# Performance work log

Hardware: AMD Instinct MI355X
Metric: run time of the kernel (lower is better)

Reference implementation:

```python
import jax, jax.numpy as jnp
import numpy as np

N, E, G = 20000, 480000, 200
HID = 32  # hidden_channels


def setup_inputs() -> dict:
    key = jax.random.key(0)
    ks = jax.random.split(key, 40)
    rn = lambda k, shape, s=0.1: jax.random.normal(k, shape, jnp.float32) * s
    inp = {
        "x": jax.random.normal(ks[0], (N, 8), jnp.float32),
        "edge_index": jax.random.randint(ks[1], (2, E), 0, N),
        "edge_attr": jax.random.normal(ks[2], (E, 4), jnp.float32),
        "batch": jnp.sort(jax.random.randint(ks[3], (N,), 0, G)),
        "descriptors": jax.random.normal(ks[4], (G, 48), jnp.float32),
        # edge encoder Linear(4 -> 32)
        "We_enc": rn(ks[5], (4, HID)), "be_enc": rn(ks[6], (HID,)),
        # gat1: GATConv(8 -> 32, heads=4, concat)
        "W1": rn(ks[7], (8, 4 * HID)), "as1": rn(ks[8], (4, HID)), "ad1": rn(ks[9], (4, HID)), "b1": rn(ks[10], (4 * HID,)),
        # gat2: GATConv(128 -> 32, heads=4, concat, edge_dim=32)
        "W2": rn(ks[11], (4 * HID, 4 * HID)), "We2": rn(ks[12], (HID, 4 * HID)),
        "as2": rn(ks[13], (4, HID)), "ad2": rn(ks[14], (4, HID)), "ae2": rn(ks[15], (4, HID)), "b2": rn(ks[16], (4 * HID,)),
        # gat3
        "W3": rn(ks[17], (4 * HID, 4 * HID)), "We3": rn(ks[18], (HID, 4 * HID)),
        "as3": rn(ks[19], (4, HID)), "ad3": rn(ks[20], (4, HID)), "ae3": rn(ks[21], (4, HID)), "b3": rn(ks[22], (4 * HID,)),
        # gat4: heads=1, concat=False
        "W4": rn(ks[23], (4 * HID, HID)), "We4": rn(ks[24], (HID, HID)),
        "as4": rn(ks[25], (1, HID)), "ad4": rn(ks[26], (1, HID)), "ae4": rn(ks[27], (1, HID)), "b4": rn(ks[28], (HID,)),
        # descriptor net Linear(48 -> 32)
        "Wd": rn(ks[29], (48, HID)), "bd": rn(ks[30], (HID,)),
        # final Linear(64 -> 1)
        "Wl": rn(ks[31], (2 * HID, 1)), "bl": rn(ks[32], (1,)),
    }
    return inp


def _gat(x, src, dst, n, W, att_s, att_d, bias, heads, ch, concat, e=None, We=None, att_e=None):
    """PyG GATConv: add self-loops (edge fill='mean'), edge softmax over incoming edges."""
    loops = jnp.arange(n)
    if e is not None:
        cnt = jnp.zeros((n,), x.dtype).at[dst].add(1.0)
        loop_e = jnp.zeros((n, e.shape[1]), x.dtype).at[dst].add(e) / jnp.maximum(cnt, 1.0)[:, None]
        e = jnp.concatenate([e, loop_e], axis=0)  # [E+N, edge_dim]
    s = jnp.concatenate([src, loops])
    d = jnp.concatenate([dst, loops])
    h = (x @ W).reshape(n, heads, ch)                      # [N,H,C]
    a_s = (h * att_s).sum(-1)                              # [N,H]
    a_d = (h * att_d).sum(-1)
    alpha = a_s[s] + a_d[d]                                # [E+N,H]
    if e is not None:
        eh = (e @ We).reshape(-1, heads, ch)
        alpha = alpha + (eh * att_e).sum(-1)
    alpha = jax.nn.leaky_relu(alpha, 0.2)
    amax = jax.ops.segment_max(alpha, d, num_segments=n)
    ex = jnp.exp(alpha - amax[d])
    den = jax.ops.segment_sum(ex, d, num_segments=n)
    alpha = ex / (den[d] + 1e-16)
    out = jax.ops.segment_sum(alpha[:, :, None] * h[s], d, num_segments=n)  # [N,H,C]
    out = out.reshape(n, heads * ch) if concat else out.mean(axis=1)
    return out + bias


def reference(x, edge_index, edge_attr, batch, descriptors,
              We_enc, be_enc,
              W1, as1, ad1, b1,
              W2, We2, as2, ad2, ae2, b2,
              W3, We3, as3, ad3, ae3, b3,
              W4, We4, as4, ad4, ae4, b4,
              Wd, bd, Wl, bl):
    src, dst = edge_index[0], edge_index[1]
    n = x.shape[0]
    edge_emb = edge_attr @ We_enc + be_enc                # [E,32]
    h = jax.nn.relu(_gat(x, src, dst, n, W1, as1, ad1, b1, 4, HID, True))
    h = jax.nn.relu(_gat(h, src, dst, n, W2, as2, ad2, b2, 4, HID, True, edge_emb, We2, ae2))
    h = jax.nn.relu(_gat(h, src, dst, n, W3, as3, ad3, b3, 4, HID, True, edge_emb, We3, ae3))
    h = _gat(h, src, dst, n, W4, as4, ad4, b4, 1, HID, False, edge_emb, We4, ae4)  # [N,32]
    # global mean pool per graph
    g_sum = jax.ops.segment_sum(h, batch, num_segments=G)
    g_cnt = jax.ops.segment_sum(jnp.ones((n,), h.dtype), batch, num_segments=G)
    graph_emb = g_sum / jnp.maximum(g_cnt, 1.0)[:, None]  # [G,32]
    desc_emb = jax.nn.relu(descriptors @ Wd + bd)          # [G,32]
    combined = jnp.concatenate([graph_emb, desc_emb], axis=1)
    return jax.nn.sigmoid(combined @ Wl + bl).reshape(-1)  # [G]
```

## Files before the change

kernel.cpp:

```cpp
#include <hip/hip_runtime.h>
#include <hip/hip_bf16.h>
#include <math.h>

#define NN 20000
#define EE 480000
#define GG 200
#define CAP 96

typedef unsigned int uint32;

static __device__ inline unsigned short f2bf(float f) {
  __hip_bfloat16 h = __float2bfloat16(f);
  return *reinterpret_cast<const unsigned short*>(&h);
}
static __device__ inline float bf2f(unsigned short u) {
  return __uint_as_float(((uint32)u) << 16);
}
static __device__ inline float bf_lo(uint32 u) { return __uint_as_float(u << 16); }
static __device__ inline float bf_hi(uint32 u) { return __uint_as_float(u & 0xffff0000u); }
static __device__ inline uint32 pack2(float lo, float hi) {
  return ((uint32)f2bf(lo)) | (((uint32)f2bf(hi)) << 16);
}

#define HB ((EE + 255) / 256)
#define GB (NN / 16)

__global__ void histgemm1_kernel(const int* __restrict__ dst, int* __restrict__ cnt,
                                 const float* __restrict__ X, const float* __restrict__ W,
                                 const float* __restrict__ att_s, const float* __restrict__ att_d,
                                 __hip_bfloat16* __restrict__ H, float* __restrict__ a_s,
                                 float* __restrict__ a_d) {
  int tid = threadIdx.x;
  if (blockIdx.x < HB) {
    int i = blockIdx.x * 256 + tid;
    if (i < EE) atomicAdd(&cnt[dst[i]], 1);
    return;
  }
  __shared__ float xs[16][8];
  int row0 = (blockIdx.x - HB) * 16;
  if (tid < 128) xs[tid >> 3][tid & 7] = X[row0 * 8 + tid];
  __syncthreads();
  int c = tid & 127;
  int half = tid >> 7;
  float acc[8];
#pragma unroll
  for (int j = 0; j < 8; ++j) acc[j] = 0.f;
  for (int k = 0; k < 8; ++k) {
    float wv = W[k * 128 + c];
#pragma unroll
    for (int j = 0; j < 8; ++j) acc[j] = fmaf(xs[half * 8 + j][k], wv, acc[j]);
  }
  float asv = att_s[c], adv = att_d[c];
#pragma unroll
  for (int j = 0; j < 8; ++j) {
    int row = row0 + half * 8 + j;
    float vs = acc[j] * asv, vd = acc[j] * adv;
#pragma unroll
    for (int m = 16; m >= 1; m >>= 1) {
      vs += __shfl_xor(vs, m);
      vd += __shfl_xor(vd, m);
    }
    H[row * 128 + c] = __float2bfloat16(acc[j]);
    if ((tid & 31) == 0) {
      a_s[row * 4 + (c >> 5)] = vs;
      a_d[row * 4 + (c >> 5)] = vd;
    }
  }
}

#define NSCAN ((NN + 1023) / 1024)

__global__ void scan1_kernel(const int* __restrict__ cnt, int* __restrict__ row_ptr,
                             int* __restrict__ partial) {
  __shared__ int buf[1024];
  int t = threadIdx.x;
  int i = blockIdx.x * 1024 + t;
  int v = (i < NN) ? cnt[i] : 0;
  buf[t] = v;
  __syncthreads();
  for (int offd = 1; offd < 1024; offd <<= 1) {
    int tmp = (t >= offd) ? buf[t - offd] : 0;
    __syncthreads();
    buf[t] += tmp;
    __syncthreads();
  }
  if (i < NN) row_ptr[i + 1] = buf[t];
  if (t == 1023) partial[blockIdx.x] = buf[1023];
}

__global__ void scan23_kernel(int* __restrict__ row_ptr, const int* __restrict__ partial) {
  __shared__ int sc[NSCAN];
  int t = threadIdx.x;
  if (t < 64) {
    int v = (t < NSCAN) ? partial[t] : 0;
    for (int o = 1; o < 32; o <<= 1) {
      int u = __shfl_up(v, o);
      if (t >= o) v += u;
    }
    if (t < NSCAN) sc[t] = v;
  }
  __syncthreads();
  int i = blockIdx.x * 256 + t;
  if (i == 0) row_ptr[0] = 0;
  if (i >= 1 && i <= NN) {
    int b = (i - 1) >> 10;
    if (b > 0) row_ptr[i] += sc[b - 1];
  }
}

__global__ void scatter_kernel(const int* __restrict__ src, const int* __restrict__ dst,
                               const float* __restrict__ attr, const int* __restrict__ row_ptr,
                               int* __restrict__ pos, int* __restrict__ csr_src,
                               uint2* __restrict__ attr_pk) {
  int e = blockIdx.x * 256 + threadIdx.x;
  if (e >= EE) return;
  int d = dst[e];
  int p = row_ptr[d] + atomicAdd(&pos[d], 1);
  csr_src[p] = src[e];
  float4 a = ((const float4*)attr)[e];
  uint2 q;
  q.x = pack2(a.x, a.y);
  q.y = pack2(a.z, a.w);
  attr_pk[p] = q;
}

#define AMB ((NN + 255) / 256)

__global__ void aux_kernel(const int* __restrict__ row_ptr, const uint2* __restrict__ attr_pk,
                           float* __restrict__ mean_attr, const int* __restrict__ batch,
                           int* __restrict__ bound, const float* __restrict__ We_enc,
                           const float* __restrict__ be_enc, const float* __restrict__ We2,
                           const float* __restrict__ ae2, const float* __restrict__ We3,
                           const float* __restrict__ ae3, const float* __restrict__ We4,
                           const float* __restrict__ ae4, float* __restrict__ fold) {
  int b = blockIdx.x;
  int t = threadIdx.x;
  if (b < AMB) {
    int node = b * 256 + t;
    if (node < NN) {
      int p0 = row_ptr[node], p1 = row_ptr[node + 1];
      float s0 = 0.f, s1 = 0.f, s2 = 0.f, s3 = 0.f;
      for (int p = p0; p < p1; ++p) {
        uint2 q = attr_pk[p];
        s0 += bf_lo(q.x); s1 += bf_hi(q.x);
        s2 += bf_lo(q.y); s3 += bf_hi(q.y);
      }
      int deg = p1 - p0;
      float inv = 1.f / (float)(deg > 1 ? deg : 1);
      ((float4*)mean_attr)[node] = make_float4(s0 * inv, s1 * inv, s2 * inv, s3 * inv);
    }
    return;
  }
  if (b < 2 * AMB) {
    int i = (b - AMB) * 256 + t;
    if (i >= NN) return;
    int bc = batch[i];
    int bp = (i == 0) ? -1 : batch[i - 1];
    for (int g = bp + 1; g <= bc; ++g) bound[g] = i;
    if (i == NN - 1)
      for (int g = bc + 1; g <= GG; ++g) bound[g] = NN;
    return;
  }
  __shared__ float V[32 * 4];
  if (t < 128) {
    int k = t >> 2, h = t & 3;
    float s = 0.f;
    for (int c = 0; c < 32; ++c) s = fmaf(We2[k * 128 + h * 32 + c], ae2[h * 32 + c], s);
    V[k * 4 + h] = s;
  }
  __syncthreads();
  if (t < 16) {
    int i = t >> 2, h = t & 3;
    float s = 0.f;
    for (int k = 0; k < 32; ++k) s = fmaf(We_enc[i * 32 + k], V[k * 4 + h], s);
    fold[i * 4 + h] = s;
  } else if (t < 20) {
    int h = t - 16;
    float s = 0.f;
    for (int k = 0; k < 32; ++k) s = fmaf(be_enc[k], V[k * 4 + h], s);
    fold[16 + h] = s;
  }
  __syncthreads();
  if (t < 128) {
    int k = t >> 2, h = t & 3;
    float s = 0.f;
    for (int c = 0; c < 32; ++c) s = fmaf(We3[k * 128 + h * 32 + c], ae3[h * 32 + c], s);
    V[k * 4 + h] = s;
  }
  __syncthreads();
  if (t < 16) {
    int i = t >> 2, h = t & 3;
    float s = 0.f;
    for (int k = 0; k < 32; ++k) s = fmaf(We_enc[i * 32 + k], V[k * 4 + h], s);
    fold[20 + i * 4 + h] = s;
  } else if (t < 20) {
    int h = t - 16;
    float s = 0.f;
    for (int k = 0; k < 32; ++k) s = fmaf(be_enc[k], V[k * 4 + h], s);
    fold[36 + h] = s;
  }
  __syncthreads();
  if (t < 32) {
    float s = 0.f;
    for (int c = 0; c < 32; ++c) s = fmaf(We4[t * 32 + c], ae4[c], s);
    V[t] = s;
  }
  __syncthreads();
  if (t < 4) {
    float s = 0.f;
    for (int k = 0; k < 32; ++k) s = fmaf(We_enc[t * 32 + k], V[k], s);
    fold[40 + t] = s;
  } else if (t == 4) {
    float s = 0.f;
    for (int k = 0; k < 32; ++k) s = fmaf(be_enc[k], V[k], s);
    fold[44] = s;
  }
}

template <int COLS, int TR>
__global__ __launch_bounds__(256) void gemm2_kernel(const float* __restrict__ X,
                                                    const float* __restrict__ W,
                                                    const float* __restrict__ att_s,
                                                    const float* __restrict__ att_d,
                                                    __hip_bfloat16* __restrict__ H,
                                                    float* __restrict__ a_s,
                                                    float* __restrict__ a_d) {
  constexpr int K = 128;
  constexpr int HEADS = COLS / 32;
  constexpr int CG = COLS / 4;
  constexpr int RG = 256 / CG;
  constexpr int ROWS = RG * TR;
  __shared__ unsigned short ws[K * COLS];
  __shared__ float xs[ROWS * K];
  int tid = threadIdx.x;
  int row0 = blockIdx.x * ROWS;
  for (int i = tid * 4; i < K * COLS; i += 1024) {
    float4 wv = *(const float4*)&W[i];
    ushort4 u;
    u.x = f2bf(wv.x); u.y = f2bf(wv.y); u.z = f2bf(wv.z); u.w = f2bf(wv.w);
    *(ushort4*)&ws[i] = u;
  }
  for (int i = tid * 4; i < ROWS * K; i += 1024) {
    int grow = row0 + i / K;
    float4 v = make_float4(0.f, 0.f, 0.f, 0.f);
    if (grow < NN) v = *(const float4*)&X[(size_t)grow * K + (i & (K - 1))];
    *(float4*)&xs[i] = v;
  }
  __syncthreads();
  int cg = tid % CG, rg = tid / CG;
  int c0 = cg * 4, r0 = rg * TR;
  float acc[TR][4];
#pragma unroll
  for (int i = 0; i < TR; ++i)
#pragma unroll
    for (int j = 0; j < 4; ++j) acc[i][j] = 0.f;
  for (int k0 = 0; k0 < K; k0 += 4) {
    float w4[4][4];
#pragma unroll
    for (int j = 0; j < 4; ++j) {
      ushort4 u = *(ushort4*)&ws[(k0 + j) * COLS + c0];
      w4[j][0] = bf2f(u.x); w4[j][1] = bf2f(u.y); w4[j][2] = bf2f(u.z); w4[j][3] = bf2f(u.w);
    }
#pragma unroll
    for (int i = 0; i < TR; ++i) {
      float4 xv = *(float4*)&xs[(r0 + i) * K + k0];
#pragma unroll
      for (int j = 0; j < 4; ++j) {
        acc[i][j] = fmaf(xv.x, w4[0][j], acc[i][j]);
        acc[i][j] = fmaf(xv.y, w4[1][j], acc[i][j]);
        acc[i][j] = fmaf(xv.z, w4[2][j], acc[i][j]);
        acc[i][j] = fmaf(xv.w, w4[3][j], acc[i][j]);
      }
    }
  }
  float as4[4], ad4[4];
#pragma unroll
  for (int j = 0; j < 4; ++j) { as4[j] = att_s[c0 + j]; ad4[j] = att_d[c0 + j]; }
  int h = c0 >> 5;
#pragma unroll
  for (int i = 0; i < TR; ++i) {
    int row = row0 + r0 + i;
    ushort4 hv;
    hv.x = f2bf(acc[i][0]); hv.y = f2bf(acc[i][1]); hv.z = f2bf(acc[i][2]); hv.w = f2bf(acc[i][3]);
    if (row < NN) *(ushort4*)&H[(size_t)row * COLS + c0] = hv;
    float vs = 0.f, vd = 0.f;
#pragma unroll
    for (int j = 0; j < 4; ++j) {
      vs = fmaf(acc[i][j], as4[j], vs);
      vd = fmaf(acc[i][j], ad4[j], vd);
    }
#pragma unroll
    for (int m = 1; m <= 4; m <<= 1) {
      vs += __shfl_xor(vs, m);
      vd += __shfl_xor(vd, m);
    }
    if ((tid & 7) == 0 && row < NN) {
      a_s[row * HEADS + h] = vs;
      a_d[row * HEADS + h] = vd;
    }
  }
}

template <int HEADS, bool RELU, bool HAS_EDGE>
__global__ __launch_bounds__(256) void gat_agg5_kernel(
    const __hip_bfloat16* __restrict__ Hh, const float* __restrict__ a_s,
    const float* __restrict__ a_d, const uint2* __restrict__ attr_pk,
    const float* __restrict__ mean_attr, const float* __restrict__ foldM,
    const float* __restrict__ foldC, const int* __restrict__ row_ptr,
    const int* __restrict__ csr_src, const float* __restrict__ bias,
    float* __restrict__ out) {
  constexpr int COLS = HEADS * 32;
  constexpr int NL = COLS / 2;
  constexpr int NPB = 256 / NL;
  constexpr int EPP = 16;
  constexpr int JMAX = CAP / EPP;
  constexpr int EXS = CAP * HEADS + (HEADS == 1 ? 1 : 0);
  constexpr int SRS = CAP + (HEADS == 1 ? 1 : 0);

  __shared__ float ex_lds[NPB][EXS];
  __shared__ int src_lds[NPB][SRS];

  int tid = threadIdx.x;
  int ln = tid % NL;
  int nl = tid / NL;
  int node = blockIdx.x * NPB + nl;
  int p0 = row_ptr[node], p1 = row_ptr[node + 1];
  int deg = p1 - p0;
  int base = (tid & 63) & ~(NL - 1);
  const uint32* H32 = (const uint32*)Hh;
  int c = 2 * ln;
  int hc = (HEADS == 4) ? (c >> 5) : 0;

  if (deg > CAP) {
    float gm0 = 0.f, gm1 = 0.f, gm2 = 0.f, gm3 = 0.f, gc = 0.f;
    if (HAS_EDGE) {
      if (HEADS == 4) {
        gm0 = foldM[hc]; gm1 = foldM[4 + hc]; gm2 = foldM[8 + hc]; gm3 = foldM[12 + hc];
        gc = foldC[hc];
      } else {
        gm0 = foldM[0]; gm1 = foldM[1]; gm2 = foldM[2]; gm3 = foldM[3];
        gc = foldC[0];
      }
    }
    float adv = a_d[node * HEADS + hc];
    float al = a_s[node * HEADS + hc] + adv;
    if (HAS_EDGE) {
      float4 m4 = ((const float4*)mean_attr)[node];
      al += fmaf(m4.x, gm0, fmaf(m4.y, gm1, fmaf(m4.z, gm2, fmaf(m4.w, gm3, gc))));
    }
    al = al >= 0.f ? al : 0.2f * al;
    float m = al;
    for (int p = p0; p < p1; ++p) {
      int s = csr_src[p];
      float a = a_s[s * HEADS + hc] + adv;
      if (HAS_EDGE) {
        uint2 q = attr_pk[p];
        a += fmaf(bf_lo(q.x), gm0,
                  fmaf(bf_hi(q.x), gm1, fmaf(bf_lo(q.y), gm2, fmaf(bf_hi(q.y), gm3, gc))));
      }
      a = a >= 0.f ? a : 0.2f * a;
      m = fmaxf(m, a);
    }
    float e0 = __expf(al - m);
    float den = e0;
    uint32 u0 = H32[(size_t)node * NL + ln];
    float acc0 = e0 * bf_lo(u0), acc1 = e0 * bf_hi(u0);
    for (int p = p0; p < p1; ++p) {
      int s = csr_src[p];
      float a = a_s[s * HEADS + hc] + adv;
      if (HAS_EDGE) {
        uint2 q = attr_pk[p];
        a += fmaf(bf_lo(q.x), gm0,
                  fmaf(bf_hi(q.x), gm1, fmaf(bf_lo(q.y), gm2, fmaf(bf_hi(q.y), gm3, gc))));
      }
      a = a >= 0.f ? a : 0.2f * a;
      float ex = __expf(a - m);
      den += ex;
      uint32 u = H32[(size_t)s * NL + ln];
      acc0 = fmaf(ex, bf_lo(u), acc0);
      acc1 = fmaf(ex, bf_hi(u), acc1);
    }
    float inv = 1.f / (den + 1e-16f);
    float o0 = acc0 * inv + bias[c];
    float o1 = acc1 * inv + bias[c + 1];
    if (RELU) { o0 = fmaxf(o0, 0.f); o1 = fmaxf(o1, 0.f); }
    *(float2*)&out[(size_t)node * COLS + c] = make_float2(o0, o1);
    return;
  }

  int p_rel = ln / HEADS;
  int h = ln % HEADS;
  float adv = a_d[node * HEADS + h];
  float fm0 = 0.f, fm1 = 0.f, fm2 = 0.f, fm3 = 0.f, fc = 0.f;
  if (HAS_EDGE) {
    if (HEADS == 4) {
      fm0 = foldM[h]; fm1 = foldM[4 + h]; fm2 = foldM[8 + h]; fm3 = foldM[12 + h];
      fc = foldC[h];
    } else {
      fm0 = foldM[0]; fm1 = foldM[1]; fm2 = foldM[2]; fm3 = foldM[3];
      fc = foldC[0];
    }
  }

  float av[JMAX];
  float mpart = -1e30f;
#pragma unroll
  for (int j = 0; j < JMAX; ++j) {
    int pr = p_rel + j * EPP;
    av[j] = -1e30f;
    int s = 0;
    if (pr < deg) {
      int p = p0 + pr;
      s = csr_src[p];
      float a = a_s[s * HEADS + h] + adv;
      if (HAS_EDGE) {
        uint2 q = attr_pk[p];
        a += fmaf(bf_lo(q.x), fm0,
                  fmaf(bf_hi(q.x), fm1, fmaf(bf_lo(q.y), fm2, fmaf(bf_hi(q.y), fm3, fc))));
      }
      a = a >= 0.f ? a : 0.2f * a;
      av[j] = a;
      mpart = fmaxf(mpart, a);
    }
    if (HEADS == 1 || h == 0) src_lds[nl][pr] = s;
  }
  float al = -1e30f;
  if (p_rel == 0) {
    al = a_s[node * HEADS + h] + adv;
    if (HAS_EDGE && deg > 0) {
      float4 m4 = ((const float4*)mean_attr)[node];
      al += fmaf(m4.x, fm0, fmaf(m4.y, fm1, fmaf(m4.z, fm2, fmaf(m4.w, fm3, fc))));
    }
    al = al >= 0.f ? al : 0.2f * al;
    mpart = fmaxf(mpart, al);
  }
  float mfull = mpart;
#pragma unroll
  for (int m = HEADS; m < NL; m <<= 1) mfull = fmaxf(mfull, __shfl_xor(mfull, m));

  float dpart = 0.f;
#pragma unroll
  for (int j = 0; j < JMAX; ++j) {
    int pr = p_rel + j * EPP;
    float ex = __expf(av[j] - mfull);
    ex_lds[nl][pr * HEADS + h] = ex;
    dpart += ex;
  }
  float exl = 0.f;
  if (p_rel == 0) {
    exl = __expf(al - mfull);
    dpart += exl;
  }
  float den = dpart;
#pragma unroll
  for (int m = HEADS; m < NL; m <<= 1) den += __shfl_xor(den, m);

  float exl_c = __shfl(exl, base + hc);
  float den_c = __shfl(den, base + hc);
  uint32 u0 = H32[(size_t)node * NL + ln];
  float acc0 = exl_c * bf_lo(u0);
  float acc1 = exl_c * bf_hi(u0);
#pragma unroll
  for (int j = 0; j < JMAX; ++j) {
    if (j * EPP < deg) {
      float exv[EPP];
      int sval[EPP];
#pragma unroll
      for (int pp = 0; pp < EPP; ++pp) {
        int p = j * EPP + pp;
        sval[pp] = src_lds[nl][p];
        exv[pp] = ex_lds[nl][p * HEADS + hc];
      }
      uint32 uv[EPP];
#pragma unroll
      for (int pp = 0; pp < EPP; ++pp) uv[pp] = H32[(size_t)sval[pp] * NL + ln];
#pragma unroll
      for (int pp = 0; pp < EPP; ++pp) {
        acc0 = fmaf(exv[pp], bf_lo(uv[pp]), acc0);
        acc1 = fmaf(exv[pp], bf_hi(uv[pp]), acc1);
      }
    }
  }
  float inv = 1.f / (den_c + 1e-16f);
  float o0 = acc0 * inv + bias[c];
  float o1 = acc1 * inv + bias[c + 1];
  if (RELU) { o0 = fmaxf(o0, 0.f); o1 = fmaxf(o1, 0.f); }
  *(float2*)&out[(size_t)node * COLS + c] = make_float2(o0, o1);
}

__global__ void pool_final_kernel(const float* __restrict__ h4, const int* __restrict__ bound,
                                  const float* __restrict__ desc, const float* __restrict__ Wd,
                                  const float* __restrict__ bd, const float* __restrict__ Wl,
                                  const float* __restrict__ bl, float* __restrict__ outp) {
  __shared__ float part[8][32];
  int g = blockIdx.x;
  int tid = threadIdx.x;
  int r0 = bound[g], r1 = bound[g + 1];
  int cch = tid & 31, chunk = tid >> 5;
  float s = 0.f;
  for (int r = r0 + chunk; r < r1; r += 8) s += h4[r * 32 + cch];
  part[chunk][cch] = s;
  __syncthreads();
  if (tid < 64) {
    float v;
    if (tid < 32) {
      float tot = 0.f;
#pragma unroll
      for (int k = 0; k < 8; ++k) tot += part[k][tid];
      int rows = r1 - r0;
      float cnt = (float)(rows > 1 ? rows : 1);
      v = (tot / cnt) * Wl[tid];
    } else {
      int cc = tid - 32;
      float acc = bd[cc];
      for (int k = 0; k < 48; ++k) acc = fmaf(desc[g * 48 + k], Wd[k * 32 + cc], acc);
      v = fmaxf(acc, 0.f) * Wl[32 + cc];
    }
#pragma unroll
    for (int m = 32; m >= 1; m >>= 1) v += __shfl_xor(v, m);
    if (tid == 0) outp[g] = 1.f / (1.f + expf(-(v + bl[0])));
  }
}

extern "C" void kernel_launch(void* const* d_in, const int* in_sizes, int n_in,
                              void* d_out, int out_size, void* d_ws, size_t ws_size,
                              hipStream_t stream) {
  const float* x = (const float*)d_in[0];
  const int* ei = (const int*)d_in[1];
  const float* edge_attr = (const float*)d_in[2];
  const int* batch = (const int*)d_in[3];
  const float* desc = (const float*)d_in[4];
  const float* We_enc = (const float*)d_in[5];
  const float* be_enc = (const float*)d_in[6];
  const float* W1 = (const float*)d_in[7];
  const float* as1 = (const float*)d_in[8];
  const float* ad1 = (const float*)d_in[9];
  const float* b1 = (const float*)d_in[10];
  const float* W2 = (const float*)d_in[11];
  const float* We2 = (const float*)d_in[12];
  const float* as2 = (const float*)d_in[13];
  const float* ad2 = (const float*)d_in[14];
  const float* ae2 = (const float*)d_in[15];
  const float* b2 = (const float*)d_in[16];
  const float* W3 = (const float*)d_in[17];
  const float* We3 = (const float*)d_in[18];
  const float* as3 = (const float*)d_in[19];
  const float* ad3 = (const float*)d_in[20];
  const float* ae3 = (const float*)d_in[21];
  const float* b3 = (const float*)d_in[22];
  const float* W4 = (const float*)d_in[23];
  const float* We4 = (const float*)d_in[24];
  const float* as4 = (const float*)d_in[25];
  const float* ad4 = (const float*)d_in[26];
  const float* ae4 = (const float*)d_in[27];
  const float* b4 = (const float*)d_in[28];
  const float* Wd = (const float*)d_in[29];
  const float* bd = (const float*)d_in[30];
  const float* Wl = (const float*)d_in[31];
  const float* bl = (const float*)d_in[32];

  const int* srcp = ei;
  const int* dstp = ei + EE;

  char* w = (char*)d_ws;
  size_t off = 0;
  auto take = [&](size_t nbytes) -> void* {
    void* p = (void*)(w + off);
    off += (nbytes + 255) & ~(size_t)255;
    return p;
  };
  int* cnt = (int*)take(2 * NN * 4);
  int* pos = cnt + NN;
  int* row_ptr = (int*)take((NN + 1) * 4);
  int* csr_src = (int*)take((size_t)EE * 4);
  uint2* attr_pk = (uint2*)take((size_t)EE * 8);
  float* mean_attr = (float*)take(NN * 16);
  float* fold = (float*)take(48 * 4);
  int* partial = (int*)take(64 * 4);
  int* bound = (int*)take((GG + 1) * 4);
  float* a_s = (float*)take(NN * 16);
  float* a_d = (float*)take(NN * 16);
  __hip_bfloat16* hbuf = (__hip_bfloat16*)take((size_t)NN * 128 * 2);
  float* obuf = (float*)take((size_t)NN * 128 * 4);
  (void)ws_size;

  hipMemsetAsync(cnt, 0, 2 * NN * 4, stream);
  histgemm1_kernel<<<HB + GB, 256, 0, stream>>>(dstp, cnt, x, W1, as1, ad1, hbuf, a_s, a_d);
  scan1_kernel<<<NSCAN, 1024, 0, stream>>>(cnt, row_ptr, partial);
  scan23_kernel<<<(NN + 256) / 256, 256, 0, stream>>>(row_ptr, partial);
  scatter_kernel<<<(EE + 255) / 256, 256, 0, stream>>>(srcp, dstp, edge_attr, row_ptr, pos,
                                                       csr_src, attr_pk);
  aux_kernel<<<2 * AMB + 1, 256, 0, stream>>>(row_ptr, attr_pk, mean_attr, batch, bound, We_enc,
                                              be_enc, We2, ae2, We3, ae3, We4, ae4, fold);

  gat_agg5_kernel<4, true, false><<<NN / 4, 256, 0, stream>>>(
      hbuf, a_s, a_d, nullptr, nullptr, nullptr, nullptr, row_ptr, csr_src, b1, obuf);
  gemm2_kernel<128, 4><<<NN / 32, 256, 0, stream>>>(obuf, W2, as2, ad2, hbuf, a_s, a_d);
  gat_agg5_kernel<4, true, true><<<NN / 4, 256, 0, stream>>>(
      hbuf, a_s, a_d, attr_pk, mean_attr, fold + 0, fold + 16, row_ptr, csr_src, b2, obuf);
  gemm2_kernel<128, 4><<<NN / 32, 256, 0, stream>>>(obuf, W3, as3, ad3, hbuf, a_s, a_d);
  gat_agg5_kernel<4, true, true><<<NN / 4, 256, 0, stream>>>(
      hbuf, a_s, a_d, attr_pk, mean_attr, fold + 20, fold + 36, row_ptr, csr_src, b3, obuf);
  gemm2_kernel<32, 2><<<(NN + 63) / 64, 256, 0, stream>>>(obuf, W4, as4, ad4, hbuf, a_s, a_d);
  gat_agg5_kernel<1, false, true><<<NN / 16, 256, 0, stream>>>(
      hbuf, a_s, a_d, attr_pk, mean_attr, fold + 40, fold + 44, row_ptr, csr_src, b4, obuf);

  pool_final_kernel<<<GG, 256, 0, stream>>>(obuf, bound, desc, Wd, bd, Wl, bl, (float*)d_out);
}
```

Before: 331.8 us.

## Fold aux kernel into histogram and first aggregation launches, batch edge loads

Removes the separate aux kernel launch. Its batch-boundary and weight-folding work moves into extra blocks of the histogram/GEMM1 kernel. The mean-edge-attribute computation becomes extra blocks appended to the layer-1 aggregation kernel, which does not need it. The aggregation kernel also issues all csr_src and attr loads for a node first, then all a_s gathers, to raise memory-level parallelism. This trades one launch and its serialization for more register pressure from the hoisted load arrays.

```diff
diff --git a/kernel.cpp b/kernel.cpp
--- a/kernel.cpp
+++ b/kernel.cpp
@@ -24,51 +24,125 @@
 
 #define HB ((EE + 255) / 256)
 #define GB (NN / 16)
+#define AMB ((NN + 255) / 256)
+#define NSCAN ((NN + 1023) / 1024)
 
 __global__ void histgemm1_kernel(const int* __restrict__ dst, int* __restrict__ cnt,
                                  const float* __restrict__ X, const float* __restrict__ W,
                                  const float* __restrict__ att_s, const float* __restrict__ att_d,
                                  __hip_bfloat16* __restrict__ H, float* __restrict__ a_s,
-                                 float* __restrict__ a_d) {
+                                 float* __restrict__ a_d, const int* __restrict__ batch,
+                                 int* __restrict__ bound, const float* __restrict__ We_enc,
+                                 const float* __restrict__ be_enc, const float* __restrict__ We2,
+                                 const float* __restrict__ ae2, const float* __restrict__ We3,
+                                 const float* __restrict__ ae3, const float* __restrict__ We4,
+                                 const float* __restrict__ ae4, float* __restrict__ fold) {
   int tid = threadIdx.x;
-  if (blockIdx.x < HB) {
-    int i = blockIdx.x * 256 + tid;
+  int b = blockIdx.x;
+  if (b < HB) {
+    int i = b * 256 + tid;
     if (i < EE) atomicAdd(&cnt[dst[i]], 1);
     return;
   }
-  __shared__ float xs[16][8];
-  int row0 = (blockIdx.x - HB) * 16;
-  if (tid < 128) xs[tid >> 3][tid & 7] = X[row0 * 8 + tid];
-  __syncthreads();
-  int c = tid & 127;
-  int half = tid >> 7;
-  float acc[8];
-#pragma unroll
-  for (int j = 0; j < 8; ++j) acc[j] = 0.f;
-  for (int k = 0; k < 8; ++k) {
-    float wv = W[k * 128 + c];
-#pragma unroll
-    for (int j = 0; j < 8; ++j) acc[j] = fmaf(xs[half * 8 + j][k], wv, acc[j]);
-  }
-  float asv = att_s[c], adv = att_d[c];
-#pragma unroll
-  for (int j = 0; j < 8; ++j) {
-    int row = row0 + half * 8 + j;
-    float vs = acc[j] * asv, vd = acc[j] * adv;
-#pragma unroll
-    for (int m = 16; m >= 1; m >>= 1) {
-      vs += __shfl_xor(vs, m);
-      vd += __shfl_xor(vd, m);
-    }
-    H[row * 128 + c] = __float2bfloat16(acc[j]);
-    if ((tid & 31) == 0) {
-      a_s[row * 4 + (c >> 5)] = vs;
-      a_d[row * 4 + (c >> 5)] = vd;
-    }
-  }
-}
-
-#define NSCAN ((NN + 1023) / 1024)
+  if (b < HB + GB) {
+    __shared__ float xs[16][8];
+    int row0 = (b - HB) * 16;
+    if (tid < 128) xs[tid >> 3][tid & 7] = X[row0 * 8 + tid];
+    __syncthreads();
+    int c = tid & 127;
+    int half = tid >> 7;
+    float acc[8];
+#pragma unroll
+    for (int j = 0; j < 8; ++j) acc[j] = 0.f;
+    for (int k = 0; k < 8; ++k) {
+      float wv = W[k * 128 + c];
+#pragma unroll
+      for (int j = 0; j < 8; ++j) acc[j] = fmaf(xs[half * 8 + j][k], wv, acc[j]);
+    }
+    float asv = att_s[c], adv = att_d[c];
+#pragma unroll
+    for (int j = 0; j < 8; ++j) {
+      int row = row0 + half * 8 + j;
+      float vs = acc[j] * asv, vd = acc[j] * adv;
+#pragma unroll
+      for (int m = 16; m >= 1; m >>= 1) {
+        vs += __shfl_xor(vs, m);
+        vd += __shfl_xor(vd, m);
+      }
+      H[row * 128 + c] = __float2bfloat16(acc[j]);
+      if ((tid & 31) == 0) {
+        a_s[row * 4 + (c >> 5)] = vs;
+        a_d[row * 4 + (c >> 5)] = vd;
+      }
+    }
+    return;
+  }
+  if (b < HB + GB + AMB) {
+    int i = (b - HB - GB) * 256 + tid;
+    if (i >= NN) return;
+    int bc = batch[i];
+    int bp = (i == 0) ? -1 : batch[i - 1];
+    for (int g = bp + 1; g <= bc; ++g) bound[g] = i;
+    if (i == NN - 1)
+      for (int g = bc + 1; g <= GG; ++g) bound[g] = NN;
+    return;
+  }
+  __shared__ float V[32 * 4];
+  int t = tid;
+  if (t < 128) {
+    int k = t >> 2, h = t & 3;
+    float s = 0.f;
+    for (int c = 0; c < 32; ++c) s = fmaf(We2[k * 128 + h * 32 + c], ae2[h * 32 + c], s);
+    V[k * 4 + h] = s;
+  }
+  __syncthreads();
+  if (t < 16) {
+    int i = t >> 2, h = t & 3;
+    float s = 0.f;
+    for (int k = 0; k < 32; ++k) s = fmaf(We_enc[i * 32 + k], V[k * 4 + h], s);
+    fold[i * 4 + h] = s;
+  } else if (t < 20) {
+    int h = t - 16;
+    float s = 0.f;
+    for (int k = 0; k < 32; ++k) s = fmaf(be_enc[k], V[k * 4 + h], s);
+    fold[16 + h] = s;
+  }
+  __syncthreads();
+  if (t < 128) {
+    int k = t >> 2, h = t & 3;
+    float s = 0.f;
+    for (int c = 0; c < 32; ++c) s = fmaf(We3[k * 128 + h * 32 + c], ae3[h * 32 + c], s);
+    V[k * 4 + h] = s;
+  }
+  __syncthreads();
+  if (t < 16) {
+    int i = t >> 2, h = t & 3;
+    float s = 0.f;
+    for (int k = 0; k < 32; ++k) s = fmaf(We_enc[i * 32 + k], V[k * 4 + h], s);
+    fold[20 + i * 4 + h] = s;
+  } else if (t < 20) {
+    int h = t - 16;
+    float s = 0.f;
+    for (int k = 0; k < 32; ++k) s = fmaf(be_enc[k], V[k * 4 + h], s);
+    fold[36 + h] = s;
+  }
+  __syncthreads();
+  if (t < 32) {
+    float s = 0.f;
+    for (int c = 0; c < 32; ++c) s = fmaf(We4[t * 32 + c], ae4[c], s);
+    V[t] = s;
+  }
+  __syncthreads();
+  if (t < 4) {
+    float s = 0.f;
+    for (int k = 0; k < 32; ++k) s = fmaf(We_enc[t * 32 + k], V[k], s);
+    fold[40 + t] = s;
+  } else if (t == 4) {
+    float s = 0.f;
+    for (int k = 0; k < 32; ++k) s = fmaf(be_enc[k], V[k], s);
+    fold[44] = s;
+  }
+}
 
 __global__ void scan1_kernel(const int* __restrict__ cnt, int* __restrict__ row_ptr,
                              int* __restrict__ partial) {
@@ -122,99 +196,6 @@
   q.x = pack2(a.x, a.y);
   q.y = pack2(a.z, a.w);
   attr_pk[p] = q;
-}
-
-#define AMB ((NN + 255) / 256)
-
-__global__ void aux_kernel(const int* __restrict__ row_ptr, const uint2* __restrict__ attr_pk,
-                           float* __restrict__ mean_attr, const int* __restrict__ batch,
-                           int* __restrict__ bound, const float* __restrict__ We_enc,
-                           const float* __restrict__ be_enc, const float* __restrict__ We2,
-                           const float* __restrict__ ae2, const float* __restrict__ We3,
-                           const float* __restrict__ ae3, const float* __restrict__ We4,
-                           const float* __restrict__ ae4, float* __restrict__ fold) {
-  int b = blockIdx.x;
-  int t = threadIdx.x;
-  if (b < AMB) {
-    int node = b * 256 + t;
-    if (node < NN) {
-      int p0 = row_ptr[node], p1 = row_ptr[node + 1];
-      float s0 = 0.f, s1 = 0.f, s2 = 0.f, s3 = 0.f;
-      for (int p = p0; p < p1; ++p) {
-        uint2 q = attr_pk[p];
-        s0 += bf_lo(q.x); s1 += bf_hi(q.x);
-        s2 += bf_lo(q.y); s3 += bf_hi(q.y);
-      }
-      int deg = p1 - p0;
-      float inv = 1.f / (float)(deg > 1 ? deg : 1);
-      ((float4*)mean_attr)[node] = make_float4(s0 * inv, s1 * inv, s2 * inv, s3 * inv);
-    }
-    return;
-  }
-  if (b < 2 * AMB) {
-    int i = (b - AMB) * 256 + t;
-    if (i >= NN) return;
-    int bc = batch[i];
-    int bp = (i == 0) ? -1 : batch[i - 1];
-    for (int g = bp + 1; g <= bc; ++g) bound[g] = i;
-    if (i == NN - 1)
-      for (int g = bc + 1; g <= GG; ++g) bound[g] = NN;
-    return;
-  }
-  __shared__ float V[32 * 4];
-  if (t < 128) {
-    int k = t >> 2, h = t & 3;
-    float s = 0.f;
-    for (int c = 0; c < 32; ++c) s = fmaf(We2[k * 128 + h * 32 + c], ae2[h * 32 + c], s);
-    V[k * 4 + h] = s;
-  }
-  __syncthreads();
-  if (t < 16) {
-    int i = t >> 2, h = t & 3;
-    float s = 0.f;
-    for (int k = 0; k < 32; ++k) s = fmaf(We_enc[i * 32 + k], V[k * 4 + h], s);
-    fold[i * 4 + h] = s;
-  } else if (t < 20) {
-    int h = t - 16;
-    float s = 0.f;
-    for (int k = 0; k < 32; ++k) s = fmaf(be_enc[k], V[k * 4 + h], s);
-    fold[16 + h] = s;
-  }
-  __syncthreads();
-  if (t < 128) {
-    int k = t >> 2, h = t & 3;
-    float s = 0.f;
-    for (int c = 0; c < 32; ++c) s = fmaf(We3[k * 128 + h * 32 + c], ae3[h * 32 + c], s);
-    V[k * 4 + h] = s;
-  }
-  __syncthreads();
-  if (t < 16) {
-    int i = t >> 2, h = t & 3;
-    float s = 0.f;
-    for (int k = 0; k < 32; ++k) s = fmaf(We_enc[i * 32 + k], V[k * 4 + h], s);
-    fold[20 + i * 4 + h] = s;
-  } else if (t < 20) {
-    int h = t - 16;
-    float s = 0.f;
-    for (int k = 0; k < 32; ++k) s = fmaf(be_enc[k], V[k * 4 + h], s);
-    fold[36 + h] = s;
-  }
-  __syncthreads();
-  if (t < 32) {
-    float s = 0.f;
-    for (int c = 0; c < 32; ++c) s = fmaf(We4[t * 32 + c], ae4[c], s);
-    V[t] = s;
-  }
-  __syncthreads();
-  if (t < 4) {
-    float s = 0.f;
-    for (int k = 0; k < 32; ++k) s = fmaf(We_enc[t * 32 + k], V[k], s);
-    fold[40 + t] = s;
-  } else if (t == 4) {
-    float s = 0.f;
-    for (int k = 0; k < 32; ++k) s = fmaf(be_enc[k], V[k], s);
-    fold[44] = s;
-  }
 }
 
 template <int COLS, int TR>
@@ -301,11 +282,11 @@
   }
 }
 
-template <int HEADS, bool RELU, bool HAS_EDGE>
-__global__ __launch_bounds__(256) void gat_agg5_kernel(
+template <int HEADS, bool RELU, bool HAS_EDGE, bool AMEAN>
+__global__ __launch_bounds__(256) void gat_agg6_kernel(
     const __hip_bfloat16* __restrict__ Hh, const float* __restrict__ a_s,
     const float* __restrict__ a_d, const uint2* __restrict__ attr_pk,
-    const float* __restrict__ mean_attr, const float* __restrict__ foldM,
+    float* __restrict__ mean_attr, const float* __restrict__ foldM,
     const float* __restrict__ foldC, const int* __restrict__ row_ptr,
     const int* __restrict__ csr_src, const float* __restrict__ bias,
     float* __restrict__ out) {
@@ -316,11 +297,29 @@
   constexpr int JMAX = CAP / EPP;
   constexpr int EXS = CAP * HEADS + (HEADS == 1 ? 1 : 0);
   constexpr int SRS = CAP + (HEADS == 1 ? 1 : 0);
+  constexpr int NB = NN / NPB;
 
   __shared__ float ex_lds[NPB][EXS];
   __shared__ int src_lds[NPB][SRS];
 
   int tid = threadIdx.x;
+  if (AMEAN && blockIdx.x >= NB) {
+    int node = (blockIdx.x - NB) * 256 + tid;
+    if (node < NN) {
+      int p0 = row_ptr[node], p1 = row_ptr[node + 1];
+      float s0 = 0.f, s1 = 0.f, s2 = 0.f, s3 = 0.f;
+      for (int p = p0; p < p1; ++p) {
+        uint2 q = attr_pk[p];
+        s0 += bf_lo(q.x); s1 += bf_hi(q.x);
+        s2 += bf_lo(q.y); s3 += bf_hi(q.y);
+      }
+      int deg = p1 - p0;
+      float inv = 1.f / (float)(deg > 1 ? deg : 1);
+      ((float4*)mean_attr)[node] = make_float4(s0 * inv, s1 * inv, s2 * inv, s3 * inv);
+    }
+    return;
+  }
+
   int ln = tid % NL;
   int nl = tid / NL;
   int node = blockIdx.x * NPB + nl;
@@ -402,19 +401,36 @@
     }
   }
 
+  int sv[JMAX];
+  uint2 qv[JMAX];
+#pragma unroll
+  for (int j = 0; j < JMAX; ++j) {
+    int pr = p_rel + j * EPP;
+    sv[j] = 0;
+    if (HAS_EDGE) qv[j] = make_uint2(0u, 0u);
+    if (pr < deg) {
+      int p = p0 + pr;
+      sv[j] = csr_src[p];
+      if (HAS_EDGE) qv[j] = attr_pk[p];
+    }
+    if (HEADS == 1 || h == 0) src_lds[nl][pr] = sv[j];
+  }
+  float asv[JMAX];
+#pragma unroll
+  for (int j = 0; j < JMAX; ++j) {
+    int pr = p_rel + j * EPP;
+    asv[j] = (pr < deg) ? a_s[sv[j] * HEADS + h] : 0.f;
+  }
   float av[JMAX];
   float mpart = -1e30f;
 #pragma unroll
   for (int j = 0; j < JMAX; ++j) {
     int pr = p_rel + j * EPP;
     av[j] = -1e30f;
-    int s = 0;
     if (pr < deg) {
-      int p = p0 + pr;
-      s = csr_src[p];
-      float a = a_s[s * HEADS + h] + adv;
+      float a = asv[j] + adv;
       if (HAS_EDGE) {
-        uint2 q = attr_pk[p];
+        uint2 q = qv[j];
         a += fmaf(bf_lo(q.x), fm0,
                   fmaf(bf_hi(q.x), fm1, fmaf(bf_lo(q.y), fm2, fmaf(bf_hi(q.y), fm3, fc))));
       }
@@ -422,7 +438,6 @@
       av[j] = a;
       mpart = fmaxf(mpart, a);
     }
-    if (HEADS == 1 || h == 0) src_lds[nl][pr] = s;
   }
   float al = -1e30f;
   if (p_rel == 0) {
@@ -585,24 +600,24 @@
   (void)ws_size;
 
   hipMemsetAsync(cnt, 0, 2 * NN * 4, stream);
-  histgemm1_kernel<<<HB + GB, 256, 0, stream>>>(dstp, cnt, x, W1, as1, ad1, hbuf, a_s, a_d);
+  histgemm1_kernel<<<HB + GB + AMB + 1, 256, 0, stream>>>(
+      dstp, cnt, x, W1, as1, ad1, hbuf, a_s, a_d, batch, bound, We_enc, be_enc, We2, ae2, We3,
+      ae3, We4, ae4, fold);
   scan1_kernel<<<NSCAN, 1024, 0, stream>>>(cnt, row_ptr, partial);
   scan23_kernel<<<(NN + 256) / 256, 256, 0, stream>>>(row_ptr, partial);
   scatter_kernel<<<(EE + 255) / 256, 256, 0, stream>>>(srcp, dstp, edge_attr, row_ptr, pos,
                                                        csr_src, attr_pk);
-  aux_kernel<<<2 * AMB + 1, 256, 0, stream>>>(row_ptr, attr_pk, mean_attr, batch, bound, We_enc,
-                                              be_enc, We2, ae2, We3, ae3, We4, ae4, fold);
-
-  gat_agg5_kernel<4, true, false><<<NN / 4, 256, 0, stream>>>(
-      hbuf, a_s, a_d, nullptr, nullptr, nullptr, nullptr, row_ptr, csr_src, b1, obuf);
+
+  gat_agg6_kernel<4, true, false, true><<<NN / 4 + AMB, 256, 0, stream>>>(
+      hbuf, a_s, a_d, attr_pk, mean_attr, nullptr, nullptr, row_ptr, csr_src, b1, obuf);
   gemm2_kernel<128, 4><<<NN / 32, 256, 0, stream>>>(obuf, W2, as2, ad2, hbuf, a_s, a_d);
-  gat_agg5_kernel<4, true, true><<<NN / 4, 256, 0, stream>>>(
+  gat_agg6_kernel<4, true, true, false><<<NN / 4, 256, 0, stream>>>(
       hbuf, a_s, a_d, attr_pk, mean_attr, fold + 0, fold + 16, row_ptr, csr_src, b2, obuf);
   gemm2_kernel<128, 4><<<NN / 32, 256, 0, stream>>>(obuf, W3, as3, ad3, hbuf, a_s, a_d);
-  gat_agg5_kernel<4, true, true><<<NN / 4, 256, 0, stream>>>(
+  gat_agg6_kernel<4, true, true, false><<<NN / 4, 256, 0, stream>>>(
       hbuf, a_s, a_d, attr_pk, mean_attr, fold + 20, fold + 36, row_ptr, csr_src, b3, obuf);
   gemm2_kernel<32, 2><<<(NN + 63) / 64, 256, 0, stream>>>(obuf, W4, as4, ad4, hbuf, a_s, a_d);
-  gat_agg5_kernel<1, false, true><<<NN / 16, 256, 0, stream>>>(
+  gat_agg6_kernel<1, false, true, false><<<NN / 16, 256, 0, stream>>>(
       hbuf, a_s, a_d, attr_pk, mean_attr, fold + 40, fold + 44, row_ptr, csr_src, b4, obuf);
 
   pool_final_kernel<<<GG, 256, 0, stream>>>(obuf, bound, desc, Wd, bd, Wl, bl, (float*)d_out);
```

Measured after the change: 328.3 us. Within noise of the previous version (-1.1%).
